# Optimization experiments

Hardware: AMD Instinct MI355X
Metric: run time of the kernel (lower is better)

Reference implementation:

```python
import jax, jax.numpy as jnp
import numpy as np

EMB = 1024
HEADS = 16
HD = EMB // HEADS

def setup_inputs() -> dict:
    key = jax.random.key(0)
    ks = jax.random.split(key, 9)
    s = 1.0 / np.sqrt(EMB)
    x = jax.random.normal(ks[0], (4, 2048, EMB), dtype=jnp.float32)
    Wq = jax.random.uniform(ks[1], (EMB, EMB), jnp.float32, -s, s)
    bq = jax.random.uniform(ks[2], (EMB,), jnp.float32, -s, s)
    Wk = jax.random.uniform(ks[3], (EMB, EMB), jnp.float32, -s, s)
    bk = jax.random.uniform(ks[4], (EMB,), jnp.float32, -s, s)
    Wv = jax.random.uniform(ks[5], (EMB, EMB), jnp.float32, -s, s)
    bv = jax.random.uniform(ks[6], (EMB,), jnp.float32, -s, s)
    Wo = jax.random.uniform(ks[7], (EMB, EMB), jnp.float32, -s, s)
    bo = jax.random.uniform(ks[8], (EMB,), jnp.float32, -s, s)
    return {"x": x, "Wq": Wq, "bq": bq, "Wk": Wk, "bk": bk, "Wv": Wv, "bv": bv, "Wo": Wo, "bo": bo}

def reference(x, Wq, bq, Wk, bk, Wv, bv, Wo, bo):
    B, T, C = x.shape
    # projections (torch Linear: y = x @ W^T + b)
    q = (x @ Wq.T + bq).reshape(B, T, HEADS, HD).transpose(0, 2, 1, 3)  # [B,H,T,hd]
    k = (x @ Wk.T + bk).reshape(B, T, HEADS, HD).transpose(0, 2, 1, 3)
    v = (x @ Wv.T + bv).reshape(B, T, HEADS, HD).transpose(0, 2, 1, 3)
    scores = jnp.einsum('bhqd,bhkd->bhqk', q, k) / jnp.sqrt(jnp.float32(HD))
    weights = jax.nn.softmax(scores, axis=-1)
    attn = jnp.einsum('bhqk,bhkd->bhqd', weights, v)
    out = attn.transpose(0, 2, 1, 3).reshape(B, T, C)
    return out @ Wo.T + bo
```

## Files before the change

kernel.cpp:

```cpp
#include <hip/hip_runtime.h>

#define TSEQ  2048
#define BATCH 4
#define NHEAD 16
#define EMB   1024

typedef __attribute__((ext_vector_type(8))) __bf16 bf16x8;
typedef __attribute__((ext_vector_type(4))) __bf16 bf16x4;
typedef __attribute__((ext_vector_type(4))) float  floatx4;

__device__ __forceinline__ void gload_lds16(const __bf16* g, __bf16* lds_uniform_base) {
  __builtin_amdgcn_global_load_lds(
      (__attribute__((address_space(1))) void*)(g),
      (__attribute__((address_space(3))) void*)(lds_uniform_base),
      16, 0, 0);
}

__global__ __launch_bounds__(256) void cvt_f32_bf16(
    const float* __restrict__ src, __bf16* __restrict__ dst)
{
  const int gid = (blockIdx.x * 256 + threadIdx.x) * 4;
  const float4 v = *(const float4*)(src + gid);
  dst[gid + 0] = (__bf16)v.x;
  dst[gid + 1] = (__bf16)v.y;
  dst[gid + 2] = (__bf16)v.z;
  dst[gid + 3] = (__bf16)v.w;
}

__global__ __launch_bounds__(256) void cvt_w4(
    const float* __restrict__ s0, const float* __restrict__ s1,
    const float* __restrict__ s2, const float* __restrict__ s3,
    __bf16* __restrict__ d0, __bf16* __restrict__ d1,
    __bf16* __restrict__ d2, __bf16* __restrict__ d3)
{
  const int z = blockIdx.z;
  const float* src = (z == 0) ? s0 : (z == 1) ? s1 : (z == 2) ? s2 : s3;
  __bf16*      dst = (z == 0) ? d0 : (z == 1) ? d1 : (z == 2) ? d2 : d3;
  const int gid = (blockIdx.x * 256 + threadIdx.x) * 4;
  const float4 v = *(const float4*)(src + gid);
  dst[gid + 0] = (__bf16)v.x;
  dst[gid + 1] = (__bf16)v.y;
  dst[gid + 2] = (__bf16)v.z;
  dst[gid + 3] = (__bf16)v.w;
}

__global__ __launch_bounds__(256) void gemm_bt_bias(
    const __bf16* __restrict__ A,
    const __bf16* __restrict__ W0, const __bf16* __restrict__ W1, const __bf16* __restrict__ W2,
    const float* __restrict__ B0, const float* __restrict__ B1, const float* __restrict__ B2,
    __bf16* __restrict__ C0, __bf16* __restrict__ C1, __bf16* __restrict__ C2)
{
  const int z = blockIdx.z;
  const __bf16* W  = (z == 0) ? W0 : ((z == 1) ? W1 : W2);
  const float*  Bb = (z == 0) ? B0 : ((z == 1) ? B1 : B2);
  __bf16*       C  = (z == 0) ? C0 : ((z == 1) ? C1 : C2);
  const float  scl = (z == 0) ? 0.125f * 1.44269504088896340736f : 1.0f;

  const int tid  = threadIdx.x;
  const int lane = tid & 63;
  const int wid  = tid >> 6;
  const int l16  = lane & 15;
  const int quad = lane >> 4;
  const int wm   = wid & 1;
  const int wn   = wid >> 1;
  const int m0   = blockIdx.y * 128;
  const int n0   = blockIdx.x * 128;

  __shared__ alignas(16) __bf16 As[128 * 32];
  __shared__ alignas(16) __bf16 Bs[128 * 32];

  floatx4 acc[4][4];
#pragma unroll
  for (int i = 0; i < 4; i++)
#pragma unroll
    for (int j = 0; j < 4; j++) acc[i][j] = (floatx4){0.f, 0.f, 0.f, 0.f};

  const int srow = tid >> 2;
  const int sseg = tid & 3;

  for (int k0 = 0; k0 < 1024; k0 += 32) {
    __syncthreads();
#pragma unroll
    for (int is = 0; is < 2; is++) {
      const int row = is * 64 + srow;
      gload_lds16(A + (size_t)(m0 + row) * 1024 + k0 + sseg * 8,
                  &As[(is * 256 + wid * 64) * 8]);
      gload_lds16(W + (size_t)(n0 + row) * 1024 + k0 + sseg * 8,
                  &Bs[(is * 256 + wid * 64) * 8]);
    }
    __syncthreads();

    bf16x8 af[4], bfr[4];
#pragma unroll
    for (int i = 0; i < 4; i++) {
      af[i]  = *(const bf16x8*)(&As[(wm * 64 + i * 16 + l16) * 32 + quad * 8]);
      bfr[i] = *(const bf16x8*)(&Bs[(wn * 64 + i * 16 + l16) * 32 + quad * 8]);
    }
#pragma unroll
    for (int i = 0; i < 4; i++)
#pragma unroll
      for (int j = 0; j < 4; j++)
        acc[i][j] = __builtin_amdgcn_mfma_f32_16x16x32_bf16(af[i], bfr[j], acc[i][j], 0, 0, 0);
  }

  float bv[4];
#pragma unroll
  for (int j = 0; j < 4; j++) bv[j] = Bb[n0 + wn * 64 + j * 16 + l16];

#pragma unroll
  for (int i = 0; i < 4; i++) {
    const size_t mrow = (size_t)m0 + wm * 64 + i * 16 + quad * 4;
#pragma unroll
    for (int j = 0; j < 4; j++) {
      const int col = n0 + wn * 64 + j * 16 + l16;
#pragma unroll
      for (int r = 0; r < 4; r++)
        C[(mrow + r) * 1024 + col] = (__bf16)((acc[i][j][r] + bv[j]) * scl);
    }
  }
}

__global__ __launch_bounds__(256) void gemm_bt_bias_f32(
    const __bf16* __restrict__ A, const __bf16* __restrict__ W,
    const float* __restrict__ Bb, float* __restrict__ C)
{
  const int tid  = threadIdx.x;
  const int lane = tid & 63;
  const int wid  = tid >> 6;
  const int l16  = lane & 15;
  const int quad = lane >> 4;
  const int wm   = wid & 1;
  const int wn   = wid >> 1;
  const int m0   = blockIdx.y * 128;
  const int n0   = blockIdx.x * 128;

  __shared__ alignas(16) __bf16 As[128 * 32];
  __shared__ alignas(16) __bf16 Bs[128 * 32];

  floatx4 acc[4][4];
#pragma unroll
  for (int i = 0; i < 4; i++)
#pragma unroll
    for (int j = 0; j < 4; j++) acc[i][j] = (floatx4){0.f, 0.f, 0.f, 0.f};

  const int srow = tid >> 2;
  const int sseg = tid & 3;

  for (int k0 = 0; k0 < 1024; k0 += 32) {
    __syncthreads();
#pragma unroll
    for (int is = 0; is < 2; is++) {
      const int row = is * 64 + srow;
      gload_lds16(A + (size_t)(m0 + row) * 1024 + k0 + sseg * 8,
                  &As[(is * 256 + wid * 64) * 8]);
      gload_lds16(W + (size_t)(n0 + row) * 1024 + k0 + sseg * 8,
                  &Bs[(is * 256 + wid * 64) * 8]);
    }
    __syncthreads();

    bf16x8 af[4], bfr[4];
#pragma unroll
    for (int i = 0; i < 4; i++) {
      af[i]  = *(const bf16x8*)(&As[(wm * 64 + i * 16 + l16) * 32 + quad * 8]);
      bfr[i] = *(const bf16x8*)(&Bs[(wn * 64 + i * 16 + l16) * 32 + quad * 8]);
    }
#pragma unroll
    for (int i = 0; i < 4; i++)
#pragma unroll
      for (int j = 0; j < 4; j++)
        acc[i][j] = __builtin_amdgcn_mfma_f32_16x16x32_bf16(af[i], bfr[j], acc[i][j], 0, 0, 0);
  }

  float bv[4];
#pragma unroll
  for (int j = 0; j < 4; j++) bv[j] = Bb[n0 + wn * 64 + j * 16 + l16];

#pragma unroll
  for (int i = 0; i < 4; i++) {
    const size_t mrow = (size_t)m0 + wm * 64 + i * 16 + quad * 4;
#pragma unroll
    for (int j = 0; j < 4; j++) {
      const int col = n0 + wn * 64 + j * 16 + l16;
#pragma unroll
      for (int r = 0; r < 4; r++)
        C[(mrow + r) * 1024 + col] = acc[i][j][r] + bv[j];
    }
  }
}

__global__ __launch_bounds__(256) void v_transpose(
    const __bf16* __restrict__ V, __bf16* __restrict__ VT)
{
  const int t0 = blockIdx.x * 64;
  const int bh = blockIdx.y;
  const int b  = bh >> 4;
  const int h  = bh & 15;
  const int tid = threadIdx.x;

  __shared__ alignas(16) __bf16 Ls[64 * 72];

  const int row = tid >> 2, seg = tid & 3;
  const __bf16* src = V + ((size_t)(b * TSEQ + t0 + row)) * EMB + h * 64;
  *(bf16x8*)(&Ls[row * 72 + seg * 8])       = *(const bf16x8*)(src + seg * 8);
  *(bf16x8*)(&Ls[row * 72 + (seg + 4) * 8]) = *(const bf16x8*)(src + (seg + 4) * 8);
  __syncthreads();

  const int od = tid >> 2, oseg = tid & 3;
  bf16x8 o0, o1;
#pragma unroll
  for (int j = 0; j < 8; j++) o0[j] = Ls[(oseg * 16 + j) * 72 + od];
#pragma unroll
  for (int j = 0; j < 8; j++) o1[j] = Ls[(oseg * 16 + 8 + j) * 72 + od];
  __bf16* dst = VT + ((size_t)bh * 64 + od) * TSEQ + t0 + oseg * 16;
  *(bf16x8*)(dst)     = o0;
  *(bf16x8*)(dst + 8) = o1;
}

__global__ __launch_bounds__(256, 4) void flash_attn(
    const __bf16* __restrict__ Q, const __bf16* __restrict__ K,
    const __bf16* __restrict__ VT, __bf16* __restrict__ O)
{
  const int qt   = blockIdx.x;
  const int bh   = blockIdx.y;
  const int b    = bh >> 4;
  const int h    = bh & 15;
  const int tid  = threadIdx.x;
  const int wid  = tid >> 6;
  const int lane = tid & 63;
  const int l16  = lane & 15;
  const int quad = lane >> 4;

  __shared__ alignas(16) __bf16 Ks[32 * 72];
  __shared__ alignas(16) __bf16 VTs[64 * 40];
  __shared__ alignas(16) __bf16 Pb[4][2][16 * 40];

  const size_t base = ((size_t)b * TSEQ) * EMB + (size_t)h * 64;
  const __bf16* qptr  = Q + base;
  const __bf16* kptr  = K + base;
  const __bf16* vtptr = VT + (size_t)bh * 64 * TSEQ;
  __bf16*       optr  = O + base;

  const int qb = qt * 128 + wid * 32;

  bf16x8 qf[2][2];
#pragma unroll
  for (int g = 0; g < 2; g++)
#pragma unroll
    for (int hf = 0; hf < 2; hf++)
      qf[g][hf] = *(const bf16x8*)(qptr + (size_t)(qb + g * 16 + l16) * EMB + hf * 32 + quad * 8);

  floatx4 Oacc[2][4];
#pragma unroll
  for (int g = 0; g < 2; g++)
#pragma unroll
    for (int dg = 0; dg < 4; dg++) Oacc[g][dg] = (floatx4){0.f, 0.f, 0.f, 0.f};
  float l_r[2] = {0.f, 0.f};

  const int krow = tid >> 3, kseg = tid & 7;
  const int vd   = tid >> 2, vseg = tid & 3;

  bf16x8 kv = *(const bf16x8*)(kptr + (size_t)krow * EMB + kseg * 8);
  bf16x8 vv = *(const bf16x8*)(vtptr + (size_t)vd * TSEQ + vseg * 8);

  for (int kt = 0; kt < TSEQ / 32; ++kt) {
    __syncthreads();
    *(bf16x8*)(&Ks[krow * 72 + kseg * 8]) = kv;
    *(bf16x8*)(&VTs[vd * 40 + vseg * 8])  = vv;
    __syncthreads();

    if (kt + 1 < TSEQ / 32) {
      kv = *(const bf16x8*)(kptr + (size_t)((kt + 1) * 32 + krow) * EMB + kseg * 8);
      vv = *(const bf16x8*)(vtptr + (size_t)vd * TSEQ + (kt + 1) * 32 + vseg * 8);
    }

    bf16x8 kf[2][2];
#pragma unroll
    for (int kg = 0; kg < 2; kg++)
#pragma unroll
      for (int hf = 0; hf < 2; hf++)
        kf[kg][hf] = *(const bf16x8*)(&Ks[(kg * 16 + l16) * 72 + hf * 32 + quad * 8]);

#pragma unroll
    for (int g = 0; g < 2; g++) {
#pragma unroll
      for (int kg = 0; kg < 2; kg++) {
        floatx4 t = (floatx4){0.f, 0.f, 0.f, 0.f};
        t = __builtin_amdgcn_mfma_f32_16x16x32_bf16(kf[kg][0], qf[g][0], t, 0, 0, 0);
        t = __builtin_amdgcn_mfma_f32_16x16x32_bf16(kf[kg][1], qf[g][1], t, 0, 0, 0);

        bf16x4 pk;
        float ps = 0.f;
#pragma unroll
        for (int r = 0; r < 4; r++) {
          const float p = exp2f(t[r]);
          ps += p;
          pk[r] = (__bf16)p;
        }
        l_r[g] += ps;
        *(bf16x4*)(&Pb[wid][g][l16 * 40 + kg * 16 + quad * 4]) = pk;
      }
    }

    __asm__ __volatile__("s_waitcnt lgkmcnt(0)" ::: "memory");

#pragma unroll
    for (int dg = 0; dg < 4; dg++) {
      const bf16x8 vf = *(const bf16x8*)(&VTs[(dg * 16 + l16) * 40 + quad * 8]);
#pragma unroll
      for (int g = 0; g < 2; g++) {
        const bf16x8 pf = *(const bf16x8*)(&Pb[wid][g][l16 * 40 + quad * 8]);
        Oacc[g][dg] = __builtin_amdgcn_mfma_f32_16x16x32_bf16(vf, pf, Oacc[g][dg], 0, 0, 0);
      }
    }
  }

#pragma unroll
  for (int g = 0; g < 2; g++) {
    float l = l_r[g];
    l += __shfl_xor(l, 16);
    l += __shfl_xor(l, 32);
    const float inv = 1.0f / l;
#pragma unroll
    for (int dg = 0; dg < 4; dg++) {
      bf16x4 ov;
#pragma unroll
      for (int r = 0; r < 4; r++) ov[r] = (__bf16)(Oacc[g][dg][r] * inv);
      *(bf16x4*)(optr + (size_t)(qb + g * 16 + l16) * EMB + dg * 16 + quad * 4) = ov;
    }
  }
}

extern "C" void kernel_launch(void* const* d_in, const int* in_sizes, int n_in,
                              void* d_out, int out_size, void* d_ws, size_t ws_size,
                              hipStream_t stream) {
  const float* x  = (const float*)d_in[0];
  const float* Wq = (const float*)d_in[1];
  const float* bq = (const float*)d_in[2];
  const float* Wk = (const float*)d_in[3];
  const float* bk = (const float*)d_in[4];
  const float* Wv = (const float*)d_in[5];
  const float* bv = (const float*)d_in[6];
  const float* Wo = (const float*)d_in[7];
  const float* bo = (const float*)d_in[8];
  float* out = (float*)d_out;

  const size_t NELEM = (size_t)BATCH * TSEQ * EMB;
  const size_t WELEM = (size_t)EMB * EMB;

  __bf16* q_b  = (__bf16*)d_out;
  __bf16* k_b  = q_b + NELEM;
  __bf16* x_b  = (__bf16*)d_ws;
  __bf16* v_b  = x_b + NELEM;
  __bf16* wq_b = v_b + NELEM;
  __bf16* wk_b = wq_b + WELEM;
  __bf16* wv_b = wk_b + WELEM;
  __bf16* wo_b = wv_b + WELEM;

  dim3 blk(256, 1, 1);

  cvt_f32_bf16<<<(int)(NELEM / 1024), blk, 0, stream>>>(x, x_b);
  cvt_w4<<<dim3((int)(WELEM / 1024), 1, 4), blk, 0, stream>>>(
      Wq, Wk, Wv, Wo, wq_b, wk_b, wv_b, wo_b);

  gemm_bt_bias<<<dim3(8, 64, 3), blk, 0, stream>>>(
      x_b, wq_b, wk_b, wv_b, bq, bk, bv, q_b, k_b, v_b);

  v_transpose<<<dim3(TSEQ / 64, BATCH * NHEAD), blk, 0, stream>>>(v_b, x_b);

  flash_attn<<<dim3(TSEQ / 128, BATCH * NHEAD), blk, 0, stream>>>(q_b, k_b, x_b, v_b);

  gemm_bt_bias_f32<<<dim3(8, 64, 1), blk, 0, stream>>>(v_b, wo_b, bo, out);
}
```

Measured before the change: 316.2 us.

## Double-buffer K/V tiles in flash attention with 512-thread blocks

The flash attention kernel moves to 512 threads, with each wave owning 16 query rows instead of 32. K and V^T shared tiles are double-buffered, so only one barrier per step is needed and the next tile's global load overlaps compute. The first half of the threads load K and the second half load V^T. It also switches to the hardware exp2 intrinsic. Each wave now does less reuse of each K/V fragment load, which doubles LDS read traffic per FLOP; in exchange occupancy goes up and synchronisation goes down.

```diff
diff --git a/kernel.cpp b/kernel.cpp
--- a/kernel.cpp
+++ b/kernel.cpp
@@ -216,7 +216,41 @@
   *(bf16x8*)(dst + 8) = o1;
 }
 
-__global__ __launch_bounds__(256, 4) void flash_attn(
+#define FA_STEP(BUF, WRPTR, DO_WR, DO_LD, LDTILE)                                        \
+  {                                                                                      \
+    if (DO_WR) *(bf16x8*)(WRPTR) = sv;                                                   \
+    if (DO_LD) sv = *(const bf16x8*)(sptr0 + (size_t)(LDTILE) * sstep);                  \
+    _Pragma("unroll")                                                                    \
+    for (int kg = 0; kg < 2; kg++) {                                                     \
+      const bf16x8 kf0 = *(const bf16x8*)(&Ks[BUF][(kg * 16 + l16) * 72 + quad * 8]);    \
+      const bf16x8 kf1 = *(const bf16x8*)(&Ks[BUF][(kg * 16 + l16) * 72 + 32 + quad * 8]); \
+      floatx4 t = (floatx4){0.f, 0.f, 0.f, 0.f};                                         \
+      t = __builtin_amdgcn_mfma_f32_16x16x32_bf16(kf0, qf[0], t, 0, 0, 0);               \
+      t = __builtin_amdgcn_mfma_f32_16x16x32_bf16(kf1, qf[1], t, 0, 0, 0);               \
+      bf16x4 pk;                                                                         \
+      float ps = 0.f;                                                                    \
+      _Pragma("unroll")                                                                  \
+      for (int r = 0; r < 4; r++) {                                                      \
+        const float p = __builtin_amdgcn_exp2f(t[r]);                                    \
+        ps += p;                                                                         \
+        pk[r] = (__bf16)p;                                                               \
+      }                                                                                  \
+      l_r += ps;                                                                         \
+      *(bf16x4*)(&Pb[wid][l16 * 40 + kg * 16 + quad * 4]) = pk;                          \
+    }                                                                                    \
+    __asm__ __volatile__("s_waitcnt lgkmcnt(0)" ::: "memory");                           \
+    {                                                                                    \
+      const bf16x8 pf = *(const bf16x8*)(&Pb[wid][l16 * 40 + quad * 8]);                 \
+      _Pragma("unroll")                                                                  \
+      for (int dg = 0; dg < 4; dg++) {                                                   \
+        const bf16x8 vf = *(const bf16x8*)(&VTs[BUF][(dg * 16 + l16) * 40 + quad * 8]);  \
+        Oacc[dg] = __builtin_amdgcn_mfma_f32_16x16x32_bf16(vf, pf, Oacc[dg], 0, 0, 0);   \
+      }                                                                                  \
+    }                                                                                    \
+    __syncthreads();                                                                     \
+  }
+
+__global__ __launch_bounds__(512, 8) void flash_attn(
     const __bf16* __restrict__ Q, const __bf16* __restrict__ K,
     const __bf16* __restrict__ VT, __bf16* __restrict__ O)
 {
@@ -230,9 +264,9 @@
   const int l16  = lane & 15;
   const int quad = lane >> 4;
 
-  __shared__ alignas(16) __bf16 Ks[32 * 72];
-  __shared__ alignas(16) __bf16 VTs[64 * 40];
-  __shared__ alignas(16) __bf16 Pb[4][2][16 * 40];
+  __shared__ alignas(16) __bf16 Ks[2][32 * 72];
+  __shared__ alignas(16) __bf16 VTs[2][64 * 40];
+  __shared__ alignas(16) __bf16 Pb[8][16 * 40];
 
   const size_t base = ((size_t)b * TSEQ) * EMB + (size_t)h * 64;
   const __bf16* qptr  = Q + base;
@@ -240,93 +274,58 @@
   const __bf16* vtptr = VT + (size_t)bh * 64 * TSEQ;
   __bf16*       optr  = O + base;
 
-  const int qb = qt * 128 + wid * 32;
-
-  bf16x8 qf[2][2];
-#pragma unroll
-  for (int g = 0; g < 2; g++)
-#pragma unroll
-    for (int hf = 0; hf < 2; hf++)
-      qf[g][hf] = *(const bf16x8*)(qptr + (size_t)(qb + g * 16 + l16) * EMB + hf * 32 + quad * 8);
-
-  floatx4 Oacc[2][4];
-#pragma unroll
-  for (int g = 0; g < 2; g++)
-#pragma unroll
-    for (int dg = 0; dg < 4; dg++) Oacc[g][dg] = (floatx4){0.f, 0.f, 0.f, 0.f};
-  float l_r[2] = {0.f, 0.f};
-
-  const int krow = tid >> 3, kseg = tid & 7;
-  const int vd   = tid >> 2, vseg = tid & 3;
-
-  bf16x8 kv = *(const bf16x8*)(kptr + (size_t)krow * EMB + kseg * 8);
-  bf16x8 vv = *(const bf16x8*)(vtptr + (size_t)vd * TSEQ + vseg * 8);
-
-  for (int kt = 0; kt < TSEQ / 32; ++kt) {
-    __syncthreads();
-    *(bf16x8*)(&Ks[krow * 72 + kseg * 8]) = kv;
-    *(bf16x8*)(&VTs[vd * 40 + vseg * 8])  = vv;
-    __syncthreads();
-
-    if (kt + 1 < TSEQ / 32) {
-      kv = *(const bf16x8*)(kptr + (size_t)((kt + 1) * 32 + krow) * EMB + kseg * 8);
-      vv = *(const bf16x8*)(vtptr + (size_t)vd * TSEQ + (kt + 1) * 32 + vseg * 8);
-    }
-
-    bf16x8 kf[2][2];
-#pragma unroll
-    for (int kg = 0; kg < 2; kg++)
-#pragma unroll
-      for (int hf = 0; hf < 2; hf++)
-        kf[kg][hf] = *(const bf16x8*)(&Ks[(kg * 16 + l16) * 72 + hf * 32 + quad * 8]);
-
-#pragma unroll
-    for (int g = 0; g < 2; g++) {
-#pragma unroll
-      for (int kg = 0; kg < 2; kg++) {
-        floatx4 t = (floatx4){0.f, 0.f, 0.f, 0.f};
-        t = __builtin_amdgcn_mfma_f32_16x16x32_bf16(kf[kg][0], qf[g][0], t, 0, 0, 0);
-        t = __builtin_amdgcn_mfma_f32_16x16x32_bf16(kf[kg][1], qf[g][1], t, 0, 0, 0);
-
-        bf16x4 pk;
-        float ps = 0.f;
-#pragma unroll
-        for (int r = 0; r < 4; r++) {
-          const float p = exp2f(t[r]);
-          ps += p;
-          pk[r] = (__bf16)p;
-        }
-        l_r[g] += ps;
-        *(bf16x4*)(&Pb[wid][g][l16 * 40 + kg * 16 + quad * 4]) = pk;
-      }
-    }
-
-    __asm__ __volatile__("s_waitcnt lgkmcnt(0)" ::: "memory");
-
-#pragma unroll
-    for (int dg = 0; dg < 4; dg++) {
-      const bf16x8 vf = *(const bf16x8*)(&VTs[(dg * 16 + l16) * 40 + quad * 8]);
-#pragma unroll
-      for (int g = 0; g < 2; g++) {
-        const bf16x8 pf = *(const bf16x8*)(&Pb[wid][g][l16 * 40 + quad * 8]);
-        Oacc[g][dg] = __builtin_amdgcn_mfma_f32_16x16x32_bf16(vf, pf, Oacc[g][dg], 0, 0, 0);
-      }
-    }
-  }
-
-#pragma unroll
-  for (int g = 0; g < 2; g++) {
-    float l = l_r[g];
-    l += __shfl_xor(l, 16);
-    l += __shfl_xor(l, 32);
-    const float inv = 1.0f / l;
-#pragma unroll
-    for (int dg = 0; dg < 4; dg++) {
-      bf16x4 ov;
-#pragma unroll
-      for (int r = 0; r < 4; r++) ov[r] = (__bf16)(Oacc[g][dg][r] * inv);
-      *(bf16x4*)(optr + (size_t)(qb + g * 16 + l16) * EMB + dg * 16 + quad * 4) = ov;
-    }
+  const int qb = qt * 128 + wid * 16;
+
+  bf16x8 qf[2];
+#pragma unroll
+  for (int hf = 0; hf < 2; hf++)
+    qf[hf] = *(const bf16x8*)(qptr + (size_t)(qb + l16) * EMB + hf * 32 + quad * 8);
+
+  floatx4 Oacc[4];
+#pragma unroll
+  for (int dg = 0; dg < 4; dg++) Oacc[dg] = (floatx4){0.f, 0.f, 0.f, 0.f};
+  float l_r = 0.f;
+
+  const bool isK = (tid < 256);
+  const int t2   = tid & 255;
+  const int krow = t2 >> 3, kseg = t2 & 7;
+  const int vd   = t2 >> 2, vseg = t2 & 3;
+
+  const __bf16* sptr0;
+  size_t sstep;
+  __bf16 *wr0, *wr1;
+  if (isK) {
+    sptr0 = kptr + (size_t)krow * EMB + kseg * 8;
+    sstep = (size_t)32 * EMB;
+    wr0 = &Ks[0][krow * 72 + kseg * 8];
+    wr1 = &Ks[1][krow * 72 + kseg * 8];
+  } else {
+    sptr0 = vtptr + (size_t)vd * TSEQ + vseg * 8;
+    sstep = 32;
+    wr0 = &VTs[0][vd * 40 + vseg * 8];
+    wr1 = &VTs[1][vd * 40 + vseg * 8];
+  }
+
+  bf16x8 sv = *(const bf16x8*)(sptr0);
+  *(bf16x8*)wr0 = sv;
+  sv = *(const bf16x8*)(sptr0 + sstep);
+  __syncthreads();
+
+  for (int kt = 0; kt < TSEQ / 32; kt += 2) {
+    FA_STEP(0, wr1, true,                  kt + 2 < TSEQ / 32, kt + 2);
+    FA_STEP(1, wr0, kt + 2 < TSEQ / 32,    kt + 3 < TSEQ / 32, kt + 3);
+  }
+
+  float l = l_r;
+  l += __shfl_xor(l, 16);
+  l += __shfl_xor(l, 32);
+  const float inv = 1.0f / l;
+#pragma unroll
+  for (int dg = 0; dg < 4; dg++) {
+    bf16x4 ov;
+#pragma unroll
+    for (int r = 0; r < 4; r++) ov[r] = (__bf16)(Oacc[dg][r] * inv);
+    *(bf16x4*)(optr + (size_t)(qb + l16) * EMB + dg * 16 + quad * 4) = ov;
   }
 }
 
@@ -367,7 +366,8 @@
 
   v_transpose<<<dim3(TSEQ / 64, BATCH * NHEAD), blk, 0, stream>>>(v_b, x_b);
 
-  flash_attn<<<dim3(TSEQ / 128, BATCH * NHEAD), blk, 0, stream>>>(q_b, k_b, x_b, v_b);
+  flash_attn<<<dim3(TSEQ / 128, BATCH * NHEAD), dim3(512, 1, 1), 0, stream>>>(
+      q_b, k_b, x_b, v_b);
 
   gemm_bt_bias_f32<<<dim3(8, 64, 1), blk, 0, stream>>>(v_b, wo_b, bo, out);
 }
```

After: 315.0 us. No clear change (-0.4%).
